# Kernel optimization log

Measured on AMD Instinct MI355X. Metric: run time of the kernel, lower is better.

The kernel has to match this reference:

```python
import jax, jax.numpy as jnp
import numpy as np


def setup_inputs() -> dict:
    key = jax.random.key(0)
    ks = jax.random.split(key, 8)
    N, E = 100000, 3200000
    IN, H, OUT = 256, 128, 64
    x = jax.random.normal(ks[0], (N, IN), dtype=jnp.float32)
    src = jax.random.randint(ks[1], (E,), 0, N, dtype=jnp.int64)
    dst = jax.random.randint(ks[2], (E,), 0, N, dtype=jnp.int64)
    # Glorot-ish scaled weights
    W1_self = jax.random.normal(ks[3], (IN, H), dtype=jnp.float32) / np.sqrt(IN)
    W1_neigh = jax.random.normal(ks[4], (IN, H), dtype=jnp.float32) / np.sqrt(IN)
    b1 = jnp.zeros((H,), dtype=jnp.float32)
    W2_self = jax.random.normal(ks[5], (H, OUT), dtype=jnp.float32) / np.sqrt(H)
    W2_neigh = jax.random.normal(ks[6], (H, OUT), dtype=jnp.float32) / np.sqrt(H)
    b2 = jnp.zeros((OUT,), dtype=jnp.float32)
    return {"x": x, "src": src, "dst": dst,
            "W1_self": W1_self, "W1_neigh": W1_neigh, "b1": b1,
            "W2_self": W2_self, "W2_neigh": W2_neigh, "b2": b2}


def _sage_mean(h, src, dst, W_self, W_neigh, b, deg_inv):
    # mean aggregation over in-neighbors (edges src -> dst)
    N = h.shape[0]
    agg = jax.ops.segment_sum(h[src], dst, num_segments=N)  # [N, F]
    h_neigh = agg * deg_inv[:, None]
    return h @ W_self + h_neigh @ W_neigh + b


def reference(x, src, dst, W1_self, W1_neigh, b1, W2_self, W2_neigh, b2):
    N = x.shape[0]
    deg = jax.ops.segment_sum(jnp.ones_like(dst, dtype=x.dtype), dst, num_segments=N)
    deg_inv = 1.0 / jnp.maximum(deg, 1.0)  # DGL clamps in-degree to >= 1
    h = _sage_mean(x, src, dst, W1_self, W1_neigh, b1, deg_inv)
    h = jax.nn.relu(h)
    h = _sage_mean(h, src, dst, W2_self, W2_neigh, b2, deg_inv)
    return h
```

## Files before the change

kernel.cpp:

```cpp
#include <hip/hip_runtime.h>
#include <hip/hip_bf16.h>


typedef unsigned int uint32;
typedef __attribute__((ext_vector_type(8))) short short8;
typedef __attribute__((ext_vector_type(4))) float f32x4;
typedef __attribute__((ext_vector_type(2))) float f32x2;

#define NBMAX 1024
#define NQMAX 32
#define EPB   4096

#if defined(__has_builtin)
#if __has_builtin(__builtin_amdgcn_cvt_pk_f32_fp8) && __has_builtin(__builtin_amdgcn_cvt_pk_fp8_f32)
#define FP8_HW 1
#endif
#endif
#ifndef FP8_HW
#define FP8_HW 0
#endif

__device__ __forceinline__ unsigned short f2bf(float f) {
    unsigned u = __float_as_uint(f);
    u += 0x7fffu + ((u >> 16) & 1u);
    return (unsigned short)(u >> 16);
}
__device__ __forceinline__ uint32 pack2bf(float lo, float hi) {
    return (uint32)f2bf(lo) | ((uint32)f2bf(hi) << 16);
}
__device__ __forceinline__ float bf_lo(uint32 v) { return __uint_as_float(v << 16); }
__device__ __forceinline__ float bf_hi(uint32 v) { return __uint_as_float(v & 0xFFFF0000u); }

__device__ __forceinline__ unsigned char enc8(float v) {
#if FP8_HW
    return (unsigned char)(__builtin_amdgcn_cvt_pk_fp8_f32(v, v, 0, false) & 0xFF);
#else
    float g = v * 0x1p-120f;
    uint32 b = __float_as_uint(g);
    uint32 s = (b >> 24) & 0x80u;
    b &= 0x7fffffffu;
    b += 0x7ffffu + ((b >> 20) & 1u);
    int t = (int)(b >> 20) - 960;
    t = t < 0 ? 0 : (t > 126 ? 126 : t);
    return (unsigned char)(s | (uint32)t);
#endif
}
#if !FP8_HW
__device__ __forceinline__ float dec1(uint32 b) {
    uint32 bits = ((b & 0x80u) << 24) | ((b & 0x7fu) << 20);
    return __uint_as_float(bits) * 0x1p+120f;
}
#endif

template<bool HI>
__device__ __forceinline__ f32x2 cvt2(uint32 u) {
#if FP8_HW
    auto t = __builtin_amdgcn_cvt_pk_f32_fp8(u, HI);
    f32x2 r; r[0] = t[0]; r[1] = t[1];
    return r;
#else
    uint32 a = HI ? (u >> 16) : u;
    f32x2 r; r[0] = dec1(a & 0xffu); r[1] = dec1((a >> 8) & 0xffu);
    return r;
#endif
}

__device__ __forceinline__ void acc8(f32x2* acc, uint2 v) {
    acc[0] += cvt2<false>(v.x); acc[1] += cvt2<true>(v.x);
    acc[2] += cvt2<false>(v.y); acc[3] += cvt2<true>(v.y);
}

__device__ __forceinline__ f32x2 shfl_xor2(f32x2 v, int m) {
    union { f32x2 f; long long l; } u;
    u.f = v;
    u.l = __shfl_xor(u.l, m);
    return u.f;
}

__global__ __launch_bounds__(256) void k_prep(const float* __restrict__ x, uint32* __restrict__ xb,
                                              long n8, long total8, int nblk_cast,
                                              const int* __restrict__ dst, int E, int* __restrict__ bcnt,
                                              int nblk_hist,
                                              const float* __restrict__ W1s, const float* __restrict__ W1n,
                                              unsigned short* __restrict__ Wt1, int nblk_w1,
                                              const float* __restrict__ W2s, const float* __restrict__ W2n,
                                              unsigned short* __restrict__ Wt2) {
    __shared__ int hist[NBMAX];
    int b = blockIdx.x;
    if (b < nblk_cast) {
        long t = (long)b * 256 + threadIdx.x;
        if (t < total8) {
            uint4 o = make_uint4(0u, 0u, 0u, 0u);
            if (t < n8) {
                const float4* p = reinterpret_cast<const float4*>(x) + t * 2;
                float4 a = p[0], bb = p[1];
                o.x = pack2bf(a.x, a.y);  o.y = pack2bf(a.z, a.w);
                o.z = pack2bf(bb.x, bb.y); o.w = pack2bf(bb.z, bb.w);
            }
            reinterpret_cast<uint4*>(xb)[t] = o;
        }
        return;
    }
    b -= nblk_cast;
    if (b < nblk_hist) {
        for (int i = threadIdx.x; i < NBMAX; i += 256) hist[i] = 0;
        __syncthreads();
        int base = b * EPB;
        #pragma unroll 4
        for (int i = 0; i < EPB / 256; ++i) {
            int e = base + i * 256 + threadIdx.x;
            if (e < E) atomicAdd(&hist[dst[e] >> 7], 1);
        }
        __syncthreads();
        for (int i = threadIdx.x; i < NBMAX; i += 256) {
            int h = hist[i];
            if (h) atomicAdd(&bcnt[i], h);
        }
        return;
    }
    b -= nblk_hist;
    if (b < nblk_w1) {
        int t = b * 256 + threadIdx.x;
        if (t < 256 * 256) {
            int c = t >> 8, k = t & 255;
            float v = (c < 128) ? W1s[(size_t)k * 128 + c] : W1n[(size_t)k * 128 + (c - 128)];
            Wt1[t] = f2bf(v);
        }
        return;
    }
    b -= nblk_w1;
    {
        int t = b * 256 + threadIdx.x;
        if (t < 128 * 128) {
            int c = t >> 7, k = t & 127;
            float v = (c < 64) ? W2s[(size_t)k * 64 + c] : W2n[(size_t)k * 64 + (c - 64)];
            Wt2[t] = f2bf(v);
        }
    }
}

__global__ __launch_bounds__(1024) void k_scan(const int* __restrict__ bcnt, int NBF, int NQ,
                                               int* __restrict__ boffs, int* __restrict__ gfill_fine,
                                               int* __restrict__ gfillq, int E) {
    __shared__ int sd[1024];
    int tid = threadIdx.x;
    int v = (tid < NBF) ? bcnt[tid] : 0;
    sd[tid] = v;
    __syncthreads();
    for (int off = 1; off < 1024; off <<= 1) {
        int t = (tid >= off) ? sd[tid - off] : 0;
        __syncthreads();
        sd[tid] += t;
        __syncthreads();
    }
    int excl = sd[tid] - v;
    if (tid < NBF) { boffs[tid] = excl; gfill_fine[tid] = excl; }
    if (tid == 0) boffs[NBF] = E;
    __syncthreads();
    if (tid < NQ) {
        int f = tid * 32;
        gfillq[tid] = (f < NBF) ? (sd[f] - ((f < NBF) ? bcnt[f] : 0)) : E;
    }
}

__global__ __launch_bounds__(256) void k_scatter_coarse(const int* __restrict__ src,
                                                        const int* __restrict__ dst, int E,
                                                        int* __restrict__ gfillq,
                                                        uint32* __restrict__ pairs1) {
    __shared__ int hist[NQMAX];
    __shared__ int basea[NQMAX];
    if (threadIdx.x < NQMAX) hist[threadIdx.x] = 0;
    __syncthreads();
    int base = blockIdx.x * EPB;
    #pragma unroll 4
    for (int i = 0; i < EPB / 256; ++i) {
        int e = base + i * 256 + threadIdx.x;
        if (e < E) atomicAdd(&hist[dst[e] >> 12], 1);
    }
    __syncthreads();
    if (threadIdx.x < NQMAX) {
        int h = hist[threadIdx.x];
        basea[threadIdx.x] = h ? atomicAdd(&gfillq[threadIdx.x], h) : 0;
        hist[threadIdx.x] = 0;
    }
    __syncthreads();
    #pragma unroll 4
    for (int i = 0; i < EPB / 256; ++i) {
        int e = base + i * 256 + threadIdx.x;
        if (e < E) {
            int d = dst[e];
            int q = d >> 12;
            int pos = basea[q] + atomicAdd(&hist[q], 1);
            pairs1[pos] = ((uint32)src[e] << 12) | (uint32)(d & 4095);
        }
    }
}

__global__ __launch_bounds__(256) void k_scatter_fine(const uint32* __restrict__ pairs1,
                                                      const int* __restrict__ boffs,
                                                      const int* __restrict__ qend,
                                                      int* __restrict__ gfill_fine,
                                                      uint32* __restrict__ pairs2, int NC) {
    __shared__ int hist[32];
    __shared__ int basea[32];
    const int q = blockIdx.x;
    const int s0 = boffs[q * 32];
    const int s1 = qend[q];
    for (long cb = (long)s0 + (long)blockIdx.y * EPB; cb < s1; cb += (long)NC * EPB) {
        int cend = (int)((cb + EPB < s1) ? cb + EPB : s1);
        if (threadIdx.x < 32) hist[threadIdx.x] = 0;
        __syncthreads();
        for (int e = (int)cb + threadIdx.x; e < cend; e += 256)
            atomicAdd(&hist[(pairs1[e] >> 7) & 31], 1);
        __syncthreads();
        if (threadIdx.x < 32) {
            int h = hist[threadIdx.x];
            basea[threadIdx.x] = h ? atomicAdd(&gfill_fine[q * 32 + threadIdx.x], h) : 0;
            hist[threadIdx.x] = 0;
        }
        __syncthreads();
        for (int e = (int)cb + threadIdx.x; e < cend; e += 256) {
            uint32 p = pairs1[e];
            int fl = (p >> 7) & 31;
            int pos = basea[fl] + atomicAdd(&hist[fl], 1);
            pairs2[pos] = p;
        }
        __syncthreads();
    }
}

__global__ __launch_bounds__(256) void k_bucket_sort(const uint32* __restrict__ pairs,
                                                     const int* __restrict__ boffs,
                                                     int N, int E,
                                                     int* __restrict__ row_start,
                                                     float* __restrict__ deg_inv,
                                                     int* __restrict__ src_sorted) {
    __shared__ int cnt[128];
    __shared__ int sc[128];
    __shared__ int fill[128];
    int b = blockIdx.x, tid = threadIdx.x;
    int s0 = boffs[b], s1 = boffs[b + 1];
    if (tid < 128) cnt[tid] = 0;
    __syncthreads();
    for (int e = s0 + tid; e < s1; e += 256)
        atomicAdd(&cnt[pairs[e] & 127], 1);
    __syncthreads();
    if (tid < 128) sc[tid] = cnt[tid];
    __syncthreads();
    for (int off = 1; off < 128; off <<= 1) {
        int v = 0;
        if (tid < 128 && tid >= off) v = sc[tid - off];
        __syncthreads();
        if (tid < 128) sc[tid] += v;
        __syncthreads();
    }
    if (tid < 128) {
        int excl = sc[tid] - cnt[tid];
        int node = b * 128 + tid;
        if (node < N) {
            row_start[node] = s0 + excl;
            int d = cnt[tid];
            deg_inv[node] = 1.0f / (float)(d > 1 ? d : 1);
        }
        fill[tid] = s0 + excl;
    }
    if (b == 0 && tid == 0) row_start[N] = E;
    __syncthreads();
    for (int e = s0 + tid; e < s1; e += 256) {
        uint32 p = pairs[e];
        int pos = atomicAdd(&fill[p & 127], 1);
        src_sorted[pos] = (int)(p >> 12);
    }
}

template<int K, int NF, bool YSPLIT>
__global__ __launch_bounds__(512) void gemm_rs(const unsigned short* __restrict__ A, int nstrip,
                                               const unsigned short* __restrict__ Wt,
                                               unsigned short* __restrict__ S16,
                                               unsigned char* __restrict__ N8) {
    constexpr int KS = K / 32;
    __shared__ unsigned short Bs[NF * KS * 512];
    const int tid = threadIdx.x;
    const int wave = tid >> 6, lane = tid & 63;
    const int l15 = lane & 15, l4 = lane >> 4;

    const unsigned short* Wtblk = Wt + (YSPLIT ? (size_t)blockIdx.y * 128 * K : 0);
    const bool out8 = YSPLIT && (blockIdx.y == 1);

    for (int i = tid; i < NF * KS * 64; i += 512) {
        int f = i >> 6, l = i & 63;
        int s = f / NF, n = f - s * NF;
        int col = n * 16 + (l & 15);
        int k = s * 32 + (l >> 4) * 8;
        uint4 v = *reinterpret_cast<const uint4*>(&Wtblk[(size_t)col * K + k]);
        *reinterpret_cast<uint4*>(&Bs[(size_t)i * 8]) = v;
    }
    __syncthreads();

    const unsigned short* Bl = Bs + (size_t)lane * 8;
    const int stride = gridDim.x;
    int g = blockIdx.x;
    if (g >= nstrip) return;

    uint4 uA[KS], uB[KS];

    auto loadA = [&](int gg, uint4* u) {
        int arow = gg * 128 + wave * 16 + l15;
        const unsigned short* Ar = A + (size_t)arow * K + l4 * 8;
        #pragma unroll
        for (int s = 0; s < KS; ++s)
            u[s] = *reinterpret_cast<const uint4*>(Ar + s * 32);
    };

    auto compute = [&](int gc, uint4* u) {
        f32x4 acc[NF] = {};
        #pragma unroll
        for (int s = 0; s < KS; ++s) {
            union { uint4 q; short8 v; } cv;
            cv.q = u[s];
            short8 af = cv.v;
            #pragma unroll
            for (int n = 0; n < NF; ++n) {
                short8 bf = *reinterpret_cast<const short8*>(Bl + (size_t)(s * NF + n) * 512);
                acc[n] = __builtin_amdgcn_mfma_f32_16x16x32_bf16(af, bf, acc[n], 0, 0, 0);
            }
        }
        const int rbase = gc * 128 + wave * 16;
        #pragma unroll
        for (int n = 0; n < NF; ++n) {
            #pragma unroll
            for (int r = 0; r < 4; ++r) {
                int rw = rbase + l4 * 4 + r;
                if constexpr (YSPLIT) {
                    int col = n * 16 + l15;
                    if (out8) N8[(size_t)rw * 128 + col] = enc8(acc[n][r]);
                    else      S16[(size_t)rw * 128 + col] = f2bf(acc[n][r]);
                } else {
                    if (n < 4) S16[(size_t)rw * 64 + n * 16 + l15] = f2bf(acc[n][r]);
                    else       N8[(size_t)rw * 64 + (n - 4) * 16 + l15] = enc8(acc[n][r]);
                }
            }
        }
    };

    loadA(g, uA);
    while (true) {
        int gn = g + stride;
        if (gn < nstrip) loadA(gn, uB);
        compute(g, uA);
        if (gn >= nstrip) break;
        g = gn;
        gn = g + stride;
        if (gn < nstrip) loadA(gn, uA);
        compute(g, uB);
        if (gn >= nstrip) break;
        g = gn;
    }
}

__global__ __launch_bounds__(256) void k_agg1(const uint2* __restrict__ t1n, const uint4* __restrict__ t1s,
                                              const int* __restrict__ rs, const int* __restrict__ ss,
                                              const float* __restrict__ dinv, const float* __restrict__ b1,
                                              uint4* __restrict__ h, int N) {
    int wid  = (blockIdx.x * blockDim.x + threadIdx.x) >> 6;
    int lane = threadIdx.x & 63;
    if (wid >= N) return;
    int e0 = rs[wid], e1 = rs[wid + 1];
    const int q = lane >> 4, c = lane & 15;
    f32x2 acc[4] = {};
    int e = e0;
    for (; e + 16 <= e1; e += 16) {
        int s0 = ss[e + q];
        int s1 = ss[e + 4 + q];
        int s2 = ss[e + 8 + q];
        int s3 = ss[e + 12 + q];
        uint2 v0 = t1n[(size_t)s0 * 16 + c];
        uint2 v1 = t1n[(size_t)s1 * 16 + c];
        uint2 v2 = t1n[(size_t)s2 * 16 + c];
        uint2 v3 = t1n[(size_t)s3 * 16 + c];
        acc8(acc, v0); acc8(acc, v1); acc8(acc, v2); acc8(acc, v3);
    }
    for (; e < e1; e += 4) {
        if (e + q < e1) {
            uint2 v = t1n[(size_t)ss[e + q] * 16 + c];
            acc8(acc, v);
        }
    }
    #pragma unroll
    for (int j = 0; j < 4; ++j) {
        acc[j] += shfl_xor2(acc[j], 16);
        acc[j] += shfl_xor2(acc[j], 32);
    }
    if (lane < 16) {
        float di = dinv[wid];
        uint4 sv = t1s[(size_t)wid * 16 + c];
        float4 bA = *reinterpret_cast<const float4*>(&b1[c * 8]);
        float4 bB = *reinterpret_cast<const float4*>(&b1[c * 8 + 4]);
        float h0 = fmaxf(fmaf(acc[0][0], di, bf_lo(sv.x)) + bA.x, 0.f);
        float h1 = fmaxf(fmaf(acc[0][1], di, bf_hi(sv.x)) + bA.y, 0.f);
        float h2 = fmaxf(fmaf(acc[1][0], di, bf_lo(sv.y)) + bA.z, 0.f);
        float h3 = fmaxf(fmaf(acc[1][1], di, bf_hi(sv.y)) + bA.w, 0.f);
        float h4 = fmaxf(fmaf(acc[2][0], di, bf_lo(sv.z)) + bB.x, 0.f);
        float h5 = fmaxf(fmaf(acc[2][1], di, bf_hi(sv.z)) + bB.y, 0.f);
        float h6 = fmaxf(fmaf(acc[3][0], di, bf_lo(sv.w)) + bB.z, 0.f);
        float h7 = fmaxf(fmaf(acc[3][1], di, bf_hi(sv.w)) + bB.w, 0.f);
        uint4 o;
        o.x = pack2bf(h0, h1); o.y = pack2bf(h2, h3);
        o.z = pack2bf(h4, h5); o.w = pack2bf(h6, h7);
        h[(size_t)wid * 16 + c] = o;
    }
}

__global__ __launch_bounds__(256) void k_agg2(const uint2* __restrict__ t2n, const uint4* __restrict__ t2s,
                                              const int* __restrict__ rs, const int* __restrict__ ss,
                                              const float* __restrict__ dinv, const float* __restrict__ b2,
                                              float* __restrict__ out, int N) {
    int wid  = (blockIdx.x * blockDim.x + threadIdx.x) >> 6;
    int lane = threadIdx.x & 63;
    if (wid >= N) return;
    int e0 = rs[wid], e1 = rs[wid + 1];
    const int q = lane >> 3, c = lane & 7;
    f32x2 acc[4] = {};
    int e = e0;
    for (; e + 32 <= e1; e += 32) {
        int s0 = ss[e + q];
        int s1 = ss[e + 8 + q];
        int s2 = ss[e + 16 + q];
        int s3 = ss[e + 24 + q];
        uint2 v0 = t2n[(size_t)s0 * 8 + c];
        uint2 v1 = t2n[(size_t)s1 * 8 + c];
        uint2 v2 = t2n[(size_t)s2 * 8 + c];
        uint2 v3 = t2n[(size_t)s3 * 8 + c];
        acc8(acc, v0); acc8(acc, v1); acc8(acc, v2); acc8(acc, v3);
    }
    for (; e < e1; e += 8) {
        if (e + q < e1) {
            uint2 v = t2n[(size_t)ss[e + q] * 8 + c];
            acc8(acc, v);
        }
    }
    #pragma unroll
    for (int j = 0; j < 4; ++j) {
        acc[j] += shfl_xor2(acc[j], 8);
        acc[j] += shfl_xor2(acc[j], 16);
        acc[j] += shfl_xor2(acc[j], 32);
    }
    if (lane < 8) {
        float di = dinv[wid];
        uint4 sv = t2s[(size_t)wid * 8 + c];
        float4 bA = *reinterpret_cast<const float4*>(&b2[c * 8]);
        float4 bB = *reinterpret_cast<const float4*>(&b2[c * 8 + 4]);
        float4 oA, oB;
        oA.x = fmaf(acc[0][0], di, bf_lo(sv.x)) + bA.x;
        oA.y = fmaf(acc[0][1], di, bf_hi(sv.x)) + bA.y;
        oA.z = fmaf(acc[1][0], di, bf_lo(sv.y)) + bA.z;
        oA.w = fmaf(acc[1][1], di, bf_hi(sv.y)) + bA.w;
        oB.x = fmaf(acc[2][0], di, bf_lo(sv.z)) + bB.x;
        oB.y = fmaf(acc[2][1], di, bf_hi(sv.z)) + bB.y;
        oB.z = fmaf(acc[3][0], di, bf_lo(sv.w)) + bB.z;
        oB.w = fmaf(acc[3][1], di, bf_hi(sv.w)) + bB.w;
        *reinterpret_cast<float4*>(&out[(size_t)wid * 64 + c * 8]) = oA;
        *reinterpret_cast<float4*>(&out[(size_t)wid * 64 + c * 8 + 4]) = oB;
    }
}

extern "C" void kernel_launch(void* const* d_in, const int* in_sizes, int n_in,
                              void* d_out, int out_size, void* d_ws, size_t ws_size,
                              hipStream_t stream) {
    const float* x   = (const float*)d_in[0];
    const int*   src = (const int*)d_in[1];
    const int*   dst = (const int*)d_in[2];
    const float* W1s = (const float*)d_in[3];
    const float* W1n = (const float*)d_in[4];
    const float* b1  = (const float*)d_in[5];
    const float* W2s = (const float*)d_in[6];
    const float* W2n = (const float*)d_in[7];
    const float* b2  = (const float*)d_in[8];
    float* out = (float*)d_out;

    const int IN = 256, H = 128, OUT = 64;
    const int N  = in_sizes[0] / IN;
    const int E  = in_sizes[1];
    const int Mpad = (N + 127) & ~127;
    const int NBF = (N + 127) >> 7;
    const int NQ  = (N + 4095) >> 12;

    char* ws = (char*)d_ws;
    size_t off = 0;
    auto alloc = [&](size_t bytes) -> char* {
        char* p = ws + off;
        off = (off + bytes + 255) & ~(size_t)255;
        return p;
    };
    int*   row_start  = (int*)  alloc((size_t)(N + 1) * 4);
    float* deg_inv    = (float*)alloc((size_t)N * 4);
    int*   bcnt       = (int*)  alloc((size_t)NBMAX * 4);
    int*   boffs      = (int*)  alloc((size_t)(NBMAX + 1) * 4);
    int*   gfill_fine = (int*)  alloc((size_t)NBMAX * 4);
    int*   gfillq     = (int*)  alloc((size_t)NQMAX * 4);
    int*   src_sorted = (int*)  alloc((size_t)E * 4);
    uint32* pairs1    = (uint32*)alloc((size_t)E * 4);
    uint32* pairs2    = (uint32*)alloc((size_t)E * 4);
    unsigned short* xb  = (unsigned short*)alloc((size_t)Mpad * IN * 2);
    unsigned short* Wt1 = (unsigned short*)alloc((size_t)(2 * H) * IN * 2);
    unsigned short* Wt2 = (unsigned short*)alloc((size_t)(2 * OUT) * H * 2);
    unsigned short* t1s = (unsigned short*)alloc((size_t)Mpad * H * 2);
    unsigned char*  t1n = (unsigned char*) alloc((size_t)Mpad * H);
    unsigned short* hbf = (unsigned short*)alloc((size_t)Mpad * H * 2);

    hipMemsetAsync(bcnt, 0, (size_t)NBMAX * 4, stream);
    long n8 = (long)N * IN / 8, total8 = (long)Mpad * IN / 8;
    int nblk_cast = (int)((total8 + 255) / 256);
    int nblk_hist = (E + EPB - 1) / EPB;
    int nblk_w1   = (2 * H * IN + 255) / 256;
    int nblk_w2   = (2 * OUT * H + 255) / 256;
    k_prep<<<nblk_cast + nblk_hist + nblk_w1 + nblk_w2, 256, 0, stream>>>(
        x, (uint32*)xb, n8, total8, nblk_cast,
        dst, E, bcnt, nblk_hist,
        W1s, W1n, Wt1, nblk_w1,
        W2s, W2n, Wt2);

    k_scan          <<<1, 1024, 0, stream>>>(bcnt, NBF, NQ, boffs, gfill_fine, gfillq, E);
    k_scatter_coarse<<<nblk_hist, 256, 0, stream>>>(src, dst, E, gfillq, pairs1);
    k_scatter_fine  <<<dim3(NQ, 32), 256, 0, stream>>>(pairs1, boffs, gfillq, gfill_fine, pairs2, 32);
    k_bucket_sort   <<<NBF, 256, 0, stream>>>(pairs2, boffs, N, E, row_start, deg_inv, src_sorted);

    int nstrip1 = Mpad / 128;
    int gx1 = (nstrip1 + 1) / 2;
    gemm_rs<256, 8, true><<<dim3(gx1, 2), 512, 0, stream>>>(xb, nstrip1, Wt1, t1s, t1n);
    k_agg1<<<(N + 3) / 4, 256, 0, stream>>>((const uint2*)t1n, (const uint4*)t1s,
                                            row_start, src_sorted, deg_inv, b1, (uint4*)hbf, N);
    int nstrip2 = Mpad / 128;
    int gx2 = (nstrip2 + 1) / 2;
    gemm_rs<128, 8, false><<<dim3(gx2, 1), 512, 0, stream>>>(hbf, nstrip2, Wt2, t1s, t1n);
    k_agg2<<<(N + 3) / 4, 256, 0, stream>>>((const uint2*)t1n, (const uint4*)t1s,
                                            row_start, src_sorted, deg_inv, b2, out, N);
}
```

Baseline: 302.0 us.

## Split layer-1 GEMM into four 64-column tiles with triple-buffered A loads

The layer-1 GEMM is specialised into its own kernel. The output columns are split across four grid y-slices of 64 columns each, instead of two slices of 128, which halves the B tile in LDS and the accumulator count per thread. A third register buffer prefetches A strips three iterations ahead, and launch bounds ask for higher occupancy, to hide global load latency. The trade-off is that each A strip is now read by four blocks instead of two, roughly doubling A reads, and the deeper prefetch adds register pressure. The layer-2 GEMM is copied unchanged into a separate kernel.

```diff
diff --git a/kernel.cpp b/kernel.cpp
--- a/kernel.cpp
+++ b/kernel.cpp
@@ -273,23 +273,24 @@
     }
 }
 
-template<int K, int NF, bool YSPLIT>
-__global__ __launch_bounds__(512) void gemm_rs(const unsigned short* __restrict__ A, int nstrip,
-                                               const unsigned short* __restrict__ Wt,
-                                               unsigned short* __restrict__ S16,
-                                               unsigned char* __restrict__ N8) {
-    constexpr int KS = K / 32;
+__global__ __launch_bounds__(512, 4) void gemm_l1(const unsigned short* __restrict__ A, int nstrip,
+                                                  const unsigned short* __restrict__ Wt,
+                                                  unsigned short* __restrict__ S16,
+                                                  unsigned char* __restrict__ N8) {
+    constexpr int K = 256, KS = 8, NF = 4;
     __shared__ unsigned short Bs[NF * KS * 512];
     const int tid = threadIdx.x;
     const int wave = tid >> 6, lane = tid & 63;
     const int l15 = lane & 15, l4 = lane >> 4;
 
-    const unsigned short* Wtblk = Wt + (YSPLIT ? (size_t)blockIdx.y * 128 * K : 0);
-    const bool out8 = YSPLIT && (blockIdx.y == 1);
+    const int ycol = blockIdx.y * 64;
+    const unsigned short* Wtblk = Wt + (size_t)ycol * K;
+    const bool out8 = blockIdx.y >= 2;
+    const int colbase = (blockIdx.y & 1) * 64;
 
     for (int i = tid; i < NF * KS * 64; i += 512) {
         int f = i >> 6, l = i & 63;
-        int s = f / NF, n = f - s * NF;
+        int s = f >> 2, n = f & 3;
         int col = n * 16 + (l & 15);
         int k = s * 32 + (l >> 4) * 8;
         uint4 v = *reinterpret_cast<const uint4*>(&Wtblk[(size_t)col * K + k]);
@@ -298,11 +299,11 @@
     __syncthreads();
 
     const unsigned short* Bl = Bs + (size_t)lane * 8;
-    const int stride = gridDim.x;
+    const int st = gridDim.x;
     int g = blockIdx.x;
     if (g >= nstrip) return;
 
-    uint4 uA[KS], uB[KS];
+    uint4 uA[KS], uB[KS], uC[KS];
 
     auto loadA = [&](int gg, uint4* u) {
         int arow = gg * 128 + wave * 16 + l15;
@@ -328,17 +329,88 @@
         const int rbase = gc * 128 + wave * 16;
         #pragma unroll
         for (int n = 0; n < NF; ++n) {
+            int col = colbase + n * 16 + l15;
             #pragma unroll
             for (int r = 0; r < 4; ++r) {
                 int rw = rbase + l4 * 4 + r;
-                if constexpr (YSPLIT) {
-                    int col = n * 16 + l15;
-                    if (out8) N8[(size_t)rw * 128 + col] = enc8(acc[n][r]);
-                    else      S16[(size_t)rw * 128 + col] = f2bf(acc[n][r]);
-                } else {
-                    if (n < 4) S16[(size_t)rw * 64 + n * 16 + l15] = f2bf(acc[n][r]);
-                    else       N8[(size_t)rw * 64 + (n - 4) * 16 + l15] = enc8(acc[n][r]);
-                }
+                if (out8) N8[(size_t)rw * 128 + col] = enc8(acc[n][r]);
+                else      S16[(size_t)rw * 128 + col] = f2bf(acc[n][r]);
+            }
+        }
+    };
+
+    loadA(g, uA);
+    if (g + st < nstrip) loadA(g + st, uB);
+    if (g + 2 * st < nstrip) loadA(g + 2 * st, uC);
+    while (true) {
+        compute(g, uA);
+        { int gp = g + 3 * st; if (gp < nstrip) loadA(gp, uA); }
+        g += st; if (g >= nstrip) break;
+        compute(g, uB);
+        { int gp = g + 3 * st; if (gp < nstrip) loadA(gp, uB); }
+        g += st; if (g >= nstrip) break;
+        compute(g, uC);
+        { int gp = g + 3 * st; if (gp < nstrip) loadA(gp, uC); }
+        g += st; if (g >= nstrip) break;
+    }
+}
+
+__global__ __launch_bounds__(512) void gemm_l2(const unsigned short* __restrict__ A, int nstrip,
+                                               const unsigned short* __restrict__ Wt,
+                                               unsigned short* __restrict__ S16,
+                                               unsigned char* __restrict__ N8) {
+    constexpr int K = 128, KS = 4, NF = 8;
+    __shared__ unsigned short Bs[NF * KS * 512];
+    const int tid = threadIdx.x;
+    const int wave = tid >> 6, lane = tid & 63;
+    const int l15 = lane & 15, l4 = lane >> 4;
+
+    for (int i = tid; i < NF * KS * 64; i += 512) {
+        int f = i >> 6, l = i & 63;
+        int s = f / NF, n = f - s * NF;
+        int col = n * 16 + (l & 15);
+        int k = s * 32 + (l >> 4) * 8;
+        uint4 v = *reinterpret_cast<const uint4*>(&Wt[(size_t)col * K + k]);
+        *reinterpret_cast<uint4*>(&Bs[(size_t)i * 8]) = v;
+    }
+    __syncthreads();
+
+    const unsigned short* Bl = Bs + (size_t)lane * 8;
+    const int stride = gridDim.x;
+    int g = blockIdx.x;
+    if (g >= nstrip) return;
+
+    uint4 uA[KS], uB[KS];
+
+    auto loadA = [&](int gg, uint4* u) {
+        int arow = gg * 128 + wave * 16 + l15;
+        const unsigned short* Ar = A + (size_t)arow * K + l4 * 8;
+        #pragma unroll
+        for (int s = 0; s < KS; ++s)
+            u[s] = *reinterpret_cast<const uint4*>(Ar + s * 32);
+    };
+
+    auto compute = [&](int gc, uint4* u) {
+        f32x4 acc[NF] = {};
+        #pragma unroll
+        for (int s = 0; s < KS; ++s) {
+            union { uint4 q; short8 v; } cv;
+            cv.q = u[s];
+            short8 af = cv.v;
+            #pragma unroll
+            for (int n = 0; n < NF; ++n) {
+                short8 bf = *reinterpret_cast<const short8*>(Bl + (size_t)(s * NF + n) * 512);
+                acc[n] = __builtin_amdgcn_mfma_f32_16x16x32_bf16(af, bf, acc[n], 0, 0, 0);
+            }
+        }
+        const int rbase = gc * 128 + wave * 16;
+        #pragma unroll
+        for (int n = 0; n < NF; ++n) {
+            #pragma unroll
+            for (int r = 0; r < 4; ++r) {
+                int rw = rbase + l4 * 4 + r;
+                if (n < 4) S16[(size_t)rw * 64 + n * 16 + l15] = f2bf(acc[n][r]);
+                else       N8[(size_t)rw * 64 + (n - 4) * 16 + l15] = enc8(acc[n][r]);
             }
         }
     };
@@ -526,13 +598,13 @@
     k_bucket_sort   <<<NBF, 256, 0, stream>>>(pairs2, boffs, N, E, row_start, deg_inv, src_sorted);
 
     int nstrip1 = Mpad / 128;
-    int gx1 = (nstrip1 + 1) / 2;
-    gemm_rs<256, 8, true><<<dim3(gx1, 2), 512, 0, stream>>>(xb, nstrip1, Wt1, t1s, t1n);
+    int gx1 = (nstrip1 + 2) / 3;
+    gemm_l1<<<dim3(gx1, 4), 512, 0, stream>>>(xb, nstrip1, Wt1, t1s, t1n);
     k_agg1<<<(N + 3) / 4, 256, 0, stream>>>((const uint2*)t1n, (const uint4*)t1s,
                                             row_start, src_sorted, deg_inv, b1, (uint4*)hbf, N);
     int nstrip2 = Mpad / 128;
     int gx2 = (nstrip2 + 1) / 2;
-    gemm_rs<128, 8, false><<<dim3(gx2, 1), 512, 0, stream>>>(hbf, nstrip2, Wt2, t1s, t1n);
+    gemm_l2<<<dim3(gx2, 1), 512, 0, stream>>>(hbf, nstrip2, Wt2, t1s, t1n);
     k_agg2<<<(N + 3) / 4, 256, 0, stream>>>((const uint2*)t1n, (const uint4*)t1s,
                                             row_start, src_sorted, deg_inv, b2, out, N);
 }
```

Measured after the change: 432.0 us. +43.1%, slower.
